# Kernel tuning notes

Hardware: AMD Instinct MI355X
Metric: run time of the kernel (lower is better)

## Reference

```python
import jax, jax.numpy as jnp
import numpy as np

SOBEL_X = jnp.array([[-1., 0., 1.], [-2., 0., 2.], [-1., 0., 1.]], dtype=jnp.float32)
SOBEL_Y = jnp.array([[-1., -2., -1.], [0., 0., 0.], [1., 2., 1.]], dtype=jnp.float32)


def _aggregate_similarity_cosine(t):
    # t: [B, 2, H, W] (normalized vector field)
    z = ((0, 0), (0, 0))
    up = jnp.pad(t[:, :, 1:, :], z + ((0, 1), (0, 0)))
    down = jnp.pad(t[:, :, :-1, :], z + ((1, 0), (0, 0)))
    left = jnp.pad(t[:, :, :, 1:], z + ((0, 0), (0, 1)))
    right = jnp.pad(t[:, :, :, :-1], z + ((0, 0), (1, 0)))
    nb = jnp.stack((up, down, left, right), axis=4)          # [B,2,H,W,4]
    dp = (t[..., None] * nb).sum(axis=1)                     # [B,H,W,4]
    return jnp.stack((dp.max(axis=-1), dp.min(axis=-1)), 1)  # [B,2,H,W]


def _grad_magnitude(x):
    # depthwise 3x3 Sobel conv, SAME padding, groups=C
    C = x.shape[1]
    kx = jnp.broadcast_to(SOBEL_X[None, None], (C, 1, 3, 3))
    ky = jnp.broadcast_to(SOBEL_Y[None, None], (C, 1, 3, 3))
    dn = ('NCHW', 'OIHW', 'NCHW')
    gx = jax.lax.conv_general_dilated(x, kx, (1, 1), ((1, 1), (1, 1)),
                                      dimension_numbers=dn, feature_group_count=C)
    gy = jax.lax.conv_general_dilated(x, ky, (1, 1), ((1, 1), (1, 1)),
                                      dimension_numbers=dn, feature_group_count=C)
    return jnp.sqrt(gx * gx + gy * gy)


def setup_inputs() -> dict:
    key = jax.random.key(0)
    x = jax.random.normal(key, (16, 3, 512, 512), dtype=jnp.float32)
    return {"x": x}


def reference(x):
    e = x[:, :2]                                      # [B,2,H,W]
    delta = x[:, 2:3]                                 # [B,1,H,W]
    magnitude = jnp.linalg.norm(e, axis=1, keepdims=True)
    angle = 0.5 * jnp.arctan2(e[:, 0], e[:, 1])[:, None]
    e_norm = e / magnitude
    cross_product = e[:, 0:1] * e[:, 1:2]
    similarity = _aggregate_similarity_cosine(e_norm)  # [B,2,H,W]
    out = jnp.concatenate([e, magnitude, angle, e_norm, cross_product, delta, similarity], axis=1)  # [B,10,H,W]
    out = jnp.concatenate([out, _grad_magnitude(out)], axis=1)  # [B,20,H,W]
    return out
```

## Files before the change

### kernel.cpp

```cpp
#include <hip/hip_runtime.h>
#include <hip/hip_fp16.h>
#include <math.h>

#define IMG_H 512
#define IMG_W 512
#define NIMG  16
#define HW    (IMG_H * IMG_W)

#define TH 16
#define TW 64
#define HTH (TH + 2)
#define HTW (TW + 2)
#define ERH (TH + 4)
#define ERW (TW + 4)
#define LPH 72
#define PAD 4
#define EPS 72
#define PADE 3
#define TILES_H (IMG_H / TH)
#define TILES_W (IMG_W / TW)

typedef float vfloat4 __attribute__((ext_vector_type(4)));

__device__ __forceinline__ float rcp_fast(float v) {
#if __has_builtin(__builtin_amdgcn_rcpf)
    return __builtin_amdgcn_rcpf(v);
#else
    return 1.0f / v;
#endif
}
__device__ __forceinline__ float rsq_fast(float v) {
#if __has_builtin(__builtin_amdgcn_rsqf)
    return __builtin_amdgcn_rsqf(v);
#else
    return rsqrtf(v);
#endif
}
__device__ __forceinline__ float sqrt_fast(float v) {
#if __has_builtin(__builtin_amdgcn_sqrtf)
    return __builtin_amdgcn_sqrtf(v);
#else
    return sqrtf(v);
#endif
}

__device__ __forceinline__ float fast_atan2f(float y, float x) {
    float ay = fabsf(y), ax = fabsf(x);
    float mx = fmaxf(ay, ax), mn = fminf(ay, ax);
    float a = mn * rcp_fast(mx);
    float s = a * a;
    float r = fmaf(fmaf(fmaf(0.0208351f, s, -0.085133f), s, 0.180141f), s, -0.3302995f);
    r = a * fmaf(r, s, 0.9998660f);
    if (ay > ax)  r = 1.57079632679f - r;
    if (x < 0.0f) r = 3.14159265359f - r;
    return copysignf(r, y);
}

__device__ __forceinline__ void load4h(const __half* p, float* dst) {
    float2 raw = *reinterpret_cast<const float2*>(p);
    __half2 a = *reinterpret_cast<__half2*>(&raw.x);
    __half2 b = *reinterpret_cast<__half2*>(&raw.y);
    float2 fa = __half22float2(a), fb = __half22float2(b);
    dst[0] = fa.x; dst[1] = fa.y; dst[2] = fb.x; dst[3] = fb.y;
}

__device__ __forceinline__ void loadrow8(const __half2* p, float* a, float* b) {
    union { vfloat4 v; __half2 h[4]; } u0, u1;
    u0.v = *reinterpret_cast<const vfloat4*>(p);
    u1.v = *reinterpret_cast<const vfloat4*>(p + 4);
#pragma unroll
    for (int j = 0; j < 4; ++j) {
        float2 f = __half22float2(u0.h[j]);
        a[j] = f.x; b[j] = f.y;
    }
#pragma unroll
    for (int j = 0; j < 4; ++j) {
        float2 f = __half22float2(u1.h[j]);
        a[4 + j] = f.x; b[4 + j] = f.y;
    }
}

__device__ __forceinline__ vfloat4 sobel4(const float* tt, const float* mm, const float* bb) {
    float vs[6], dd[6];
#pragma unroll
    for (int j = 0; j < 6; ++j) {
        vs[j] = tt[j] + fmaf(2.0f, mm[j], bb[j]);
        dd[j] = bb[j] - tt[j];
    }
    vfloat4 mag;
    float gx, gy;
    gx = vs[2] - vs[0]; gy = fmaf(2.f, dd[1], dd[0] + dd[2]);
    mag.x = sqrt_fast(fmaf(gx, gx, gy * gy));
    gx = vs[3] - vs[1]; gy = fmaf(2.f, dd[2], dd[1] + dd[3]);
    mag.y = sqrt_fast(fmaf(gx, gx, gy * gy));
    gx = vs[4] - vs[2]; gy = fmaf(2.f, dd[3], dd[2] + dd[4]);
    mag.z = sqrt_fast(fmaf(gx, gx, gy * gy));
    gx = vs[5] - vs[3]; gy = fmaf(2.f, dd[4], dd[3] + dd[5]);
    mag.w = sqrt_fast(fmaf(gx, gx, gy * gy));
    return mag;
}

__global__ __launch_bounds__(256, 6) void fused_kernel(const float* __restrict__ x,
                                                       float* __restrict__ out) {
    __shared__ __align__(16) __half  lds[8][HTH * LPH];
    __shared__ __align__(16) __half2 lden[ERH * EPS];

    int bid0 = blockIdx.x;
    int bid  = (bid0 & 7) * (NIMG * TILES_H * TILES_W / 8) + (bid0 >> 3);

    int n   = bid / (TILES_H * TILES_W);
    int t   = bid - n * (TILES_H * TILES_W);
    int th  = t / TILES_W;
    int tw  = t - th * TILES_W;
    int h0  = th * TH;
    int w0  = tw * TW;

    const float* xb = x + (size_t)n * 3 * HW;
    int tid = threadIdx.x;

    for (int i = tid; i < ERH * ERW; i += 256) {
        int er = i / ERW;
        int ec = i - er * ERW;
        int h  = h0 + er - 2;
        int w  = w0 + ec - 2;
        bool inimg = (h >= 0) && (h < IMG_H) && (w >= 0) && (w < IMG_W);
        int rem = h * IMG_W + w;

        float e0 = 0.f, e1 = 0.f, en0 = 0.f, en1 = 0.f;
        if (inimg) {
            e0 = xb[rem];
            e1 = xb[HW + rem];
            float is = rsq_fast(fmaf(e0, e0, e1 * e1));
            en0 = e0 * is;
            en1 = e1 * is;
        }
        lden[er * EPS + ec + PADE] = __floats2half2_rn(en0, en1);

        int hr = er - 1, wc = ec - 1;
        if (hr >= 0 && hr < HTH && wc >= 0 && wc < HTW) {
            float dl = 0.f, m = 0.f, ang = 0.f, cp = 0.f;
            if (inimg) {
                dl = xb[2 * HW + rem];
                float s2 = fmaf(e0, e0, e1 * e1);
                m   = sqrt_fast(s2);
                ang = 0.5f * fast_atan2f(e0, e1);
                cp  = e0 * e1;
            }
            int li = hr * LPH + wc + PAD;
            lds[0][li] = __float2half(e0);
            lds[1][li] = __float2half(e1);
            lds[2][li] = __float2half(m);
            lds[3][li] = __float2half(ang);
            lds[4][li] = __float2half(cp);
            lds[5][li] = __float2half(dl);
        }
    }
    __syncthreads();

    for (int i = tid; i < HTH * HTW; i += 256) {
        int hr = i / HTW;
        int wc = i - hr * HTW;
        int eb = (hr + 1) * EPS + (wc + 1) + PADE;

        float2 o  = __half22float2(lden[eb]);
        float2 u  = __half22float2(lden[eb + EPS]);
        float2 d  = __half22float2(lden[eb - EPS]);
        float2 lf = __half22float2(lden[eb + 1]);
        float2 rg = __half22float2(lden[eb - 1]);

        float dpu = fmaf(o.x, u.x,  o.y * u.y);
        float dpd = fmaf(o.x, d.x,  o.y * d.y);
        float dpl = fmaf(o.x, lf.x, o.y * lf.y);
        float dpr = fmaf(o.x, rg.x, o.y * rg.y);

        float smax = fmaxf(fmaxf(dpu, dpd), fmaxf(dpl, dpr));
        float smin = fminf(fminf(dpu, dpd), fminf(dpl, dpr));

        int li = hr * LPH + wc + PAD;
        lds[6][li] = __float2half(smax);
        lds[7][li] = __float2half(smin);
    }
    __syncthreads();

    int r  = tid >> 4;
    int c  = tid & 15;
    int h  = h0 + r;
    int wa = w0 + 4 * c;
    float* op = out + (size_t)n * 20 * HW + (size_t)h * IMG_W + wa;

    int off = 4 * c + PAD;
    int rt = r * LPH + off;
    int rm = (r + 1) * LPH + off;
    int rb = (r + 2) * LPH + off;

    const int outch[8] = {0, 1, 2, 3, 6, 7, 8, 9};

#pragma unroll
    for (int p = 0; p < 8; ++p) {
        const __half* L = lds[p];
        float tt[8], mm[8], bb[8];
        load4h(&L[rt], tt); load4h(&L[rt + 4], tt + 4);
        load4h(&L[rm], mm); load4h(&L[rm + 4], mm + 4);
        load4h(&L[rb], bb); load4h(&L[rb + 4], bb + 4);

        vfloat4 mag = sobel4(tt, mm, bb);
        vfloat4 cen;
        cen.x = mm[1]; cen.y = mm[2]; cen.z = mm[3]; cen.w = mm[4];

        int ch = outch[p];
        __builtin_nontemporal_store(cen, reinterpret_cast<vfloat4*>(&op[(size_t)ch * HW]));
        __builtin_nontemporal_store(mag, reinterpret_cast<vfloat4*>(&op[(size_t)(10 + ch) * HW]));
    }

    {
        int eb0 = (r + 1) * EPS + 4 * c + 4;
        float ta[8], tb[8], ma[8], mb[8], ba[8], bb2[8];
        loadrow8(&lden[eb0],            ta, tb);
        loadrow8(&lden[eb0 + EPS],      ma, mb);
        loadrow8(&lden[eb0 + 2 * EPS],  ba, bb2);

        vfloat4 mag4 = sobel4(ta, ma, ba);
        vfloat4 mag5 = sobel4(tb, mb, bb2);
        vfloat4 cen4, cen5;
        cen4.x = ma[1]; cen4.y = ma[2]; cen4.z = ma[3]; cen4.w = ma[4];
        cen5.x = mb[1]; cen5.y = mb[2]; cen5.z = mb[3]; cen5.w = mb[4];

        __builtin_nontemporal_store(cen4, reinterpret_cast<vfloat4*>(&op[(size_t)4 * HW]));
        __builtin_nontemporal_store(mag4, reinterpret_cast<vfloat4*>(&op[(size_t)14 * HW]));
        __builtin_nontemporal_store(cen5, reinterpret_cast<vfloat4*>(&op[(size_t)5 * HW]));
        __builtin_nontemporal_store(mag5, reinterpret_cast<vfloat4*>(&op[(size_t)15 * HW]));
    }
}

extern "C" void kernel_launch(void* const* d_in, const int* in_sizes, int n_in,
                              void* d_out, int out_size, void* d_ws, size_t ws_size,
                              hipStream_t stream) {
    const float* x = (const float*)d_in[0];
    float* out = (float*)d_out;

    int grid = NIMG * TILES_H * TILES_W;
    fused_kernel<<<grid, 256, 0, stream>>>(x, out);
}
```

Baseline: 70.41 us.

## Pack LDS planes as half2 pairs and recompute magnitude and cross product from e

Replaces the eight separate half planes in shared memory with three interleaved half2 planes (e0/e1, angle/delta, smax/smin), so the output stage loads two channels per vectorized 16-byte row read. Magnitude and cross product are no longer stored in LDS; they are recomputed in the output stage from the fp16 e values. The normalized-vector plane's padding is realigned so its loads match the other planes, and launch bounds rise from 6 to 7 blocks per CU. Recomputing magnitude and cross product from fp16-rounded inputs can change precision slightly, and the extra recompute adds ALU work.

```diff
diff --git a/kernel.cpp b/kernel.cpp
--- a/kernel.cpp
+++ b/kernel.cpp
@@ -13,10 +13,8 @@
 #define HTW (TW + 2)
 #define ERH (TH + 4)
 #define ERW (TW + 4)
-#define LPH 72
-#define PAD 4
-#define EPS 72
-#define PADE 3
+#define SP  72
+#define PADP 4
 #define TILES_H (IMG_H / TH)
 #define TILES_W (IMG_W / TW)
 
@@ -54,14 +52,6 @@
     if (ay > ax)  r = 1.57079632679f - r;
     if (x < 0.0f) r = 3.14159265359f - r;
     return copysignf(r, y);
-}
-
-__device__ __forceinline__ void load4h(const __half* p, float* dst) {
-    float2 raw = *reinterpret_cast<const float2*>(p);
-    __half2 a = *reinterpret_cast<__half2*>(&raw.x);
-    __half2 b = *reinterpret_cast<__half2*>(&raw.y);
-    float2 fa = __half22float2(a), fb = __half22float2(b);
-    dst[0] = fa.x; dst[1] = fa.y; dst[2] = fb.x; dst[3] = fb.y;
 }
 
 __device__ __forceinline__ void loadrow8(const __half2* p, float* a, float* b) {
@@ -100,10 +90,16 @@
     return mag;
 }
 
-__global__ __launch_bounds__(256, 6) void fused_kernel(const float* __restrict__ x,
+__device__ __forceinline__ vfloat4 mk4(const float* m) {
+    vfloat4 v; v.x = m[1]; v.y = m[2]; v.z = m[3]; v.w = m[4]; return v;
+}
+
+__global__ __launch_bounds__(256, 7) void fused_kernel(const float* __restrict__ x,
                                                        float* __restrict__ out) {
-    __shared__ __align__(16) __half  lds[8][HTH * LPH];
-    __shared__ __align__(16) __half2 lden[ERH * EPS];
+    __shared__ __align__(16) __half2 lden[ERH * SP];
+    __shared__ __align__(16) __half2 pe  [HTH * SP];
+    __shared__ __align__(16) __half2 pad2[HTH * SP];
+    __shared__ __align__(16) __half2 psm [HTH * SP];
 
     int bid0 = blockIdx.x;
     int bid  = (bid0 & 7) * (NIMG * TILES_H * TILES_W / 8) + (bid0 >> 3);
@@ -134,25 +130,17 @@
             en0 = e0 * is;
             en1 = e1 * is;
         }
-        lden[er * EPS + ec + PADE] = __floats2half2_rn(en0, en1);
+        lden[er * SP + ec + PADP] = __floats2half2_rn(en0, en1);
 
         int hr = er - 1, wc = ec - 1;
         if (hr >= 0 && hr < HTH && wc >= 0 && wc < HTW) {
-            float dl = 0.f, m = 0.f, ang = 0.f, cp = 0.f;
+            float dl = 0.f, ang = 0.f;
             if (inimg) {
-                dl = xb[2 * HW + rem];
-                float s2 = fmaf(e0, e0, e1 * e1);
-                m   = sqrt_fast(s2);
+                dl  = xb[2 * HW + rem];
                 ang = 0.5f * fast_atan2f(e0, e1);
-                cp  = e0 * e1;
             }
-            int li = hr * LPH + wc + PAD;
-            lds[0][li] = __float2half(e0);
-            lds[1][li] = __float2half(e1);
-            lds[2][li] = __float2half(m);
-            lds[3][li] = __float2half(ang);
-            lds[4][li] = __float2half(cp);
-            lds[5][li] = __float2half(dl);
+            pe  [hr * SP + wc + PADP] = __floats2half2_rn(e0, e1);
+            pad2[hr * SP + wc + PADP] = __floats2half2_rn(ang, dl);
         }
     }
     __syncthreads();
@@ -160,11 +148,11 @@
     for (int i = tid; i < HTH * HTW; i += 256) {
         int hr = i / HTW;
         int wc = i - hr * HTW;
-        int eb = (hr + 1) * EPS + (wc + 1) + PADE;
+        int eb = (hr + 1) * SP + (wc + 1) + PADP;
 
         float2 o  = __half22float2(lden[eb]);
-        float2 u  = __half22float2(lden[eb + EPS]);
-        float2 d  = __half22float2(lden[eb - EPS]);
+        float2 u  = __half22float2(lden[eb + SP]);
+        float2 d  = __half22float2(lden[eb - SP]);
         float2 lf = __half22float2(lden[eb + 1]);
         float2 rg = __half22float2(lden[eb - 1]);
 
@@ -176,9 +164,7 @@
         float smax = fmaxf(fmaxf(dpu, dpd), fmaxf(dpl, dpr));
         float smin = fminf(fminf(dpu, dpd), fminf(dpl, dpr));
 
-        int li = hr * LPH + wc + PAD;
-        lds[6][li] = __float2half(smax);
-        lds[7][li] = __float2half(smin);
+        psm[hr * SP + wc + PADP] = __floats2half2_rn(smax, smin);
     }
     __syncthreads();
 
@@ -188,48 +174,72 @@
     int wa = w0 + 4 * c;
     float* op = out + (size_t)n * 20 * HW + (size_t)h * IMG_W + wa;
 
-    int off = 4 * c + PAD;
-    int rt = r * LPH + off;
-    int rm = (r + 1) * LPH + off;
-    int rb = (r + 2) * LPH + off;
-
-    const int outch[8] = {0, 1, 2, 3, 6, 7, 8, 9};
-
-#pragma unroll
-    for (int p = 0; p < 8; ++p) {
-        const __half* L = lds[p];
-        float tt[8], mm[8], bb[8];
-        load4h(&L[rt], tt); load4h(&L[rt + 4], tt + 4);
-        load4h(&L[rm], mm); load4h(&L[rm + 4], mm + 4);
-        load4h(&L[rb], bb); load4h(&L[rb + 4], bb + 4);
-
-        vfloat4 mag = sobel4(tt, mm, bb);
-        vfloat4 cen;
-        cen.x = mm[1]; cen.y = mm[2]; cen.z = mm[3]; cen.w = mm[4];
-
-        int ch = outch[p];
-        __builtin_nontemporal_store(cen, reinterpret_cast<vfloat4*>(&op[(size_t)ch * HW]));
-        __builtin_nontemporal_store(mag, reinterpret_cast<vfloat4*>(&op[(size_t)(10 + ch) * HW]));
-    }
-
-    {
-        int eb0 = (r + 1) * EPS + 4 * c + 4;
-        float ta[8], tb[8], ma[8], mb[8], ba[8], bb2[8];
-        loadrow8(&lden[eb0],            ta, tb);
-        loadrow8(&lden[eb0 + EPS],      ma, mb);
-        loadrow8(&lden[eb0 + 2 * EPS],  ba, bb2);
-
-        vfloat4 mag4 = sobel4(ta, ma, ba);
-        vfloat4 mag5 = sobel4(tb, mb, bb2);
-        vfloat4 cen4, cen5;
-        cen4.x = ma[1]; cen4.y = ma[2]; cen4.z = ma[3]; cen4.w = ma[4];
-        cen5.x = mb[1]; cen5.y = mb[2]; cen5.z = mb[3]; cen5.w = mb[4];
-
-        __builtin_nontemporal_store(cen4, reinterpret_cast<vfloat4*>(&op[(size_t)4 * HW]));
-        __builtin_nontemporal_store(mag4, reinterpret_cast<vfloat4*>(&op[(size_t)14 * HW]));
-        __builtin_nontemporal_store(cen5, reinterpret_cast<vfloat4*>(&op[(size_t)5 * HW]));
-        __builtin_nontemporal_store(mag5, reinterpret_cast<vfloat4*>(&op[(size_t)15 * HW]));
-    }
+    int pb = r * SP + 4 * c + PADP;
+    int ebn = (r + 1) * SP + 4 * c + PADP;
+
+#define NTST(CH, V) __builtin_nontemporal_store((V), reinterpret_cast<vfloat4*>(&op[(size_t)(CH) * HW]))
+
+    {
+        float ta[8], tb[8], ma[8], mb[8], ba[8], bb[8];
+        loadrow8(&pe[pb],          ta, tb);
+        loadrow8(&pe[pb + SP],     ma, mb);
+        loadrow8(&pe[pb + 2 * SP], ba, bb);
+
+        NTST(0, mk4(ma));  NTST(10, sobel4(ta, ma, ba));
+        NTST(1, mk4(mb));  NTST(11, sobel4(tb, mb, bb));
+
+        float tm[6], mm_[6], bm[6];
+#pragma unroll
+        for (int j = 0; j < 6; ++j) {
+            tm[j]  = sqrt_fast(fmaf(ta[j], ta[j], tb[j] * tb[j]));
+            mm_[j] = sqrt_fast(fmaf(ma[j], ma[j], mb[j] * mb[j]));
+            bm[j]  = sqrt_fast(fmaf(ba[j], ba[j], bb[j] * bb[j]));
+        }
+        NTST(2, mk4(mm_)); NTST(12, sobel4(tm, mm_, bm));
+
+        float tc[6], mc[6], bc[6];
+#pragma unroll
+        for (int j = 0; j < 6; ++j) {
+            tc[j] = ta[j] * tb[j];
+            mc[j] = ma[j] * mb[j];
+            bc[j] = ba[j] * bb[j];
+        }
+        NTST(6, mk4(mc));  NTST(16, sobel4(tc, mc, bc));
+    }
+
+    {
+        float ta[8], tb[8], ma[8], mb[8], ba[8], bb[8];
+        loadrow8(&pad2[pb],          ta, tb);
+        loadrow8(&pad2[pb + SP],     ma, mb);
+        loadrow8(&pad2[pb + 2 * SP], ba, bb);
+
+        NTST(3, mk4(ma));  NTST(13, sobel4(ta, ma, ba));
+        NTST(7, mk4(mb));  NTST(17, sobel4(tb, mb, bb));
+    }
+
+    {
+        float ta[8], tb[8], ma[8], mb[8], ba[8], bb[8];
+        loadrow8(&psm[pb],          ta, tb);
+        loadrow8(&psm[pb + SP],     ma, mb);
+        loadrow8(&psm[pb + 2 * SP], ba, bb);
+
+        NTST(8, mk4(ma));  NTST(18, sobel4(ta, ma, ba));
+        NTST(9, mk4(mb));  NTST(19, sobel4(tb, mb, bb));
+    }
+
+    {
+        float ta[8], tb[8], ma[8], mb[8], ba[8], bb[8];
+        loadrow8(&lden[ebn],          ta, tb);
+        loadrow8(&lden[ebn + SP],     ma, mb);
+        loadrow8(&lden[ebn + 2 * SP], ba, bb);
+
+        vfloat4 c4, c5;
+        c4.x = ma[2]; c4.y = ma[3]; c4.z = ma[4]; c4.w = ma[5];
+        c5.x = mb[2]; c5.y = mb[3]; c5.z = mb[4]; c5.w = mb[5];
+        NTST(4, c4);  NTST(14, sobel4(ta + 1, ma + 1, ba + 1));
+        NTST(5, c5);  NTST(15, sobel4(tb + 1, mb + 1, bb + 1));
+    }
+#undef NTST
 }
 
 extern "C" void kernel_launch(void* const* d_in, const int* in_sizes, int n_in,
```

Result: no change. 70.23 us (-0.3%).
